# Performance work log

Hardware: AMD Instinct MI355X
Metric: run time of the kernel (lower is better)

## Reference

```python
import jax, jax.numpy as jnp
import numpy as np

D, H, DH, DF = 128, 8, 16, 512
N_Q, N_KV, E = 20000, 20000, 640000


def _xavier(key, shape):
    fan_in, fan_out = shape[1], shape[0]
    lim = float(np.sqrt(6.0 / (fan_in + fan_out)))
    return jax.random.uniform(key, shape, jnp.float32, -lim, lim)


def layer_norm(x, g, b, eps=1e-5):
    mu = jnp.mean(x, axis=-1, keepdims=True)
    var = jnp.var(x, axis=-1, keepdims=True)
    return (x - mu) * jax.lax.rsqrt(var + eps) * g + b


def setup_inputs() -> dict:
    key = jax.random.key(0)
    ks = jax.random.split(key, 12)
    return {
        "q_feat": jax.random.normal(ks[0], (N_Q, D), jnp.float32),
        "kv_feat": jax.random.normal(ks[1], (N_KV, D), jnp.float32),
        "src": jax.random.randint(ks[2], (E,), 0, N_KV, jnp.int32),
        "dst": jax.random.randint(ks[3], (E,), 0, N_Q, jnp.int32),
        "Wq": _xavier(ks[4], (H * DH, D)),
        "Wk": _xavier(ks[5], (H * DH, D)),
        "Wv": _xavier(ks[6], (H * DH, D)),
        "Wo": _xavier(ks[7], (D, H * DH)),
        "W1": _xavier(ks[8], (DF, D)),
        "bf1": jnp.zeros((DF,), jnp.float32),
        "W2": _xavier(ks[9], (D, DF)),
        "bf2": jnp.zeros((D,), jnp.float32),
        "ln1_g": jnp.ones((D,), jnp.float32),
        "ln1_b": jnp.zeros((D,), jnp.float32),
        "ln2_g": jnp.ones((D,), jnp.float32),
        "ln2_b": jnp.zeros((D,), jnp.float32),
    }


def reference(q_feat, kv_feat, src, dst, Wq, Wk, Wv, Wo, W1, bf1, W2, bf2,
              ln1_g, ln1_b, ln2_g, ln2_b):
    n_q = q_feat.shape[0]
    # projections -> [N, H, DH]
    q = (q_feat @ Wq.T).reshape(-1, H, DH)
    k = (kv_feat @ Wk.T).reshape(-1, H, DH)
    v = (kv_feat @ Wv.T).reshape(-1, H, DH)
    # edge scores: u_mul_v then sum over d_head, scaled (score per edge per head)
    score = jnp.einsum('ehd,ehd->eh', k[src], q[dst]) / np.sqrt(DH)
    # edge_softmax grouped by destination node
    mx = jax.ops.segment_max(score, dst, num_segments=n_q)  # [Nq, H]
    ex = jnp.exp(score - mx[dst])
    denom = jax.ops.segment_sum(ex, dst, num_segments=n_q)
    att = ex / denom[dst]  # [E, H]
    # weighted scatter-sum of values to destination nodes
    msg = v[src] * att[:, :, None]  # [E, H, DH]
    out = jax.ops.segment_sum(msg, dst, num_segments=n_q)  # [Nq, H, DH]
    sa = out.reshape(n_q, H * DH) @ Wo.T
    feat = layer_norm(q_feat + sa, ln1_g, ln1_b)
    ff = jax.nn.relu(feat @ W1.T + bf1) @ W2.T + bf2
    return layer_norm(feat + ff, ln2_g, ln2_b)
```

## Files before the change

kernel.cpp:

```cpp
#include <hip/hip_runtime.h>
#include <hip/hip_fp16.h>
#include <math.h>
#include <type_traits>

#define D 128
#define NH 8
#define DHD 16
#define DF 512
#define STR 128

typedef _Float16 half8 __attribute__((ext_vector_type(8)));
typedef _Float16 half4 __attribute__((ext_vector_type(4)));
typedef float f32x4 __attribute__((ext_vector_type(4)));


__global__ __launch_bounds__(256) void mega_kernel(
    const float* __restrict__ q_feat, const float* __restrict__ kv_feat,
    const float* __restrict__ Wq, const float* __restrict__ Wk,
    const float* __restrict__ Wv,
    __half* __restrict__ fq, __half* __restrict__ fkv, int NQ, int NKV,
    const int* __restrict__ dst, const int* __restrict__ src,
    int* __restrict__ cnt, unsigned short* __restrict__ srcg, int E,
    const float* __restrict__ Wo, const float* __restrict__ W1,
    const float* __restrict__ W2,
    __half* __restrict__ wo16, __half* __restrict__ w116, __half* __restrict__ w216) {
    __shared__ __align__(16) __half As[64 * 128];
    __shared__ __align__(16) __half Ws[64 * 128];

    int xt = blockIdx.x;
    int tid = threadIdx.x;

    if (xt >= 2) {
        if (xt == (int)gridDim.x - 1) {
            int g = blockIdx.y * 256 + tid;
            if (g < 36864) {
                const float* s;
                __half* d;
                int idx = g;
                if (idx < 4096) { s = Wo; d = wo16; }
                else if (idx < 20480) { idx -= 4096; s = W1; d = w116; }
                else { idx -= 20480; s = W2; d = w216; }
                float4 f = ((const float4*)s)[idx];
                ushort4 o;
                o.x = __half_as_ushort(__float2half(f.x));
                o.y = __half_as_ushort(__float2half(f.y));
                o.z = __half_as_ushort(__float2half(f.z));
                o.w = __half_as_ushort(__float2half(f.w));
                ((ushort4*)d)[idx] = o;
            }
            return;
        }
        int b = (xt - 2) * gridDim.y + blockIdx.y;
        int i4 = b * 256 + tid;
        int base = i4 << 2;
        if (base < E) {
            int dd[4], ss[4];
            if (base + 3 < E) {
                int4 d4 = ((const int4*)dst)[i4];
                int4 s4 = ((const int4*)src)[i4];
                dd[0] = d4.x; dd[1] = d4.y; dd[2] = d4.z; dd[3] = d4.w;
                ss[0] = s4.x; ss[1] = s4.y; ss[2] = s4.z; ss[3] = s4.w;
#pragma unroll
                for (int u = 0; u < 4; ++u) {
                    int p = atomicAdd(&cnt[dd[u]], 1);
                    if (p < STR) srcg[((size_t)dd[u] << 7) + p] = (unsigned short)ss[u];
                }
            } else {
                for (int u = 0; u < 4 && base + u < E; ++u) {
                    int dn = dst[base + u];
                    int sn = src[base + u];
                    int p = atomicAdd(&cnt[dn], 1);
                    if (p < STR) srcg[((size_t)dn << 7) + p] = (unsigned short)sn;
                }
            }
        }
        return;
    }

    const float* A = xt ? kv_feat : q_feat;
    __half* C = xt ? fkv : fq;
    int O = xt ? 256 : 128;
    int NCT = xt ? 4 : 2;
    int N = xt ? NKV : NQ;
    int row0 = blockIdx.y * 64;
    if (row0 >= N) return;

    int lane = tid & 63;
    int w = tid >> 6;
    int l16 = lane & 15, lq = lane >> 4;

#pragma unroll
    for (int i = 0; i < 4; ++i) {
        int f = tid + i * 256;
        int ln = f & 63;
        int mt = (f >> 6) & 3;
        int kc = f >> 8;
        int m = row0 + mt * 16 + (ln & 15);
        int k = kc * 32 + (ln >> 4) * 8;
        half8 v = {};
        if (m < N) {
            const float4* p = (const float4*)(A + (size_t)m * 128 + k);
            float4 f0 = p[0], f1 = p[1];
            v = (half8){(_Float16)f0.x, (_Float16)f0.y, (_Float16)f0.z, (_Float16)f0.w,
                        (_Float16)f1.x, (_Float16)f1.y, (_Float16)f1.z, (_Float16)f1.w};
        }
        ((half8*)As)[f] = v;
    }

    for (int ct = 0; ct < NCT; ++ct) {
        __syncthreads();
#pragma unroll
        for (int i = 0; i < 4; ++i) {
            int f = tid + i * 256;
            int ln = f & 63;
            int nt = (f >> 6) & 3;
            int kc = f >> 8;
            int n = ct * 64 + nt * 16 + (ln & 15);
            int k = kc * 32 + (ln >> 4) * 8;
            const float* Wsrc;
            int r;
            if (xt == 0) {
                Wsrc = Wq; r = n;
            } else {
                int h = n >> 5, qd = (n >> 3) & 3, isv = (n >> 2) & 1, d2 = n & 3;
                r = h * 16 + qd * 4 + d2;
                Wsrc = isv ? Wv : Wk;
            }
            const float4* p = (const float4*)(Wsrc + (size_t)r * 128 + k);
            float4 f0 = p[0], f1 = p[1];
            ((half8*)Ws)[f] = (half8){(_Float16)f0.x, (_Float16)f0.y, (_Float16)f0.z, (_Float16)f0.w,
                                      (_Float16)f1.x, (_Float16)f1.y, (_Float16)f1.z, (_Float16)f1.w};
        }
        __syncthreads();
        f32x4 acc[4];
#pragma unroll
        for (int j = 0; j < 4; ++j) acc[j] = (f32x4){0.f, 0.f, 0.f, 0.f};
#pragma unroll
        for (int kc = 0; kc < 4; ++kc) {
            half8 a = ((half8*)As)[(kc * 4 + w) * 64 + lane];
            half8 b[4];
#pragma unroll
            for (int j = 0; j < 4; ++j) b[j] = ((half8*)Ws)[(kc * 4 + j) * 64 + lane];
#pragma unroll
            for (int j = 0; j < 4; ++j)
                acc[j] = __builtin_amdgcn_mfma_f32_16x16x32_f16(a, b[j], acc[j], 0, 0, 0);
        }
#pragma unroll
        for (int j = 0; j < 4; ++j) {
            int c = ct * 64 + j * 16 + l16;
#pragma unroll
            for (int r = 0; r < 4; ++r) {
                int row = row0 + w * 16 + lq * 4 + r;
                if (row < N) C[(size_t)row * O + c] = __float2half(acc[j][r]);
            }
        }
    }
}


__global__ __launch_bounds__(256) void attn_kernel(
    const __half* __restrict__ q, const __half* __restrict__ kv,
    const unsigned short* __restrict__ srcg, const int* __restrict__ cnt,
    __half* __restrict__ out, int NQ) {
    int n = blockIdx.x * 4 + (threadIdx.x >> 6);
    if (n >= NQ) return;
    int lane = threadIdx.x & 63;
    int eh = lane >> 5;
    int sub = lane & 31;
    int doff = sub << 2;
    half4 q4 = *(const half4*)(q + (size_t)n * D + doff);
    float q0 = (float)q4[0] * 0.25f, q1 = (float)q4[1] * 0.25f;
    float q2 = (float)q4[2] * 0.25f, q3 = (float)q4[3] * 0.25f;
    int s0 = n << 7;
    int c_ = cnt[n];
    int s1 = s0 + (c_ < STR ? c_ : STR);
    float lA = 0.f, lB = 0.f, lC = 0.f, lD = 0.f;
    f32x4 aA = {0.f, 0.f, 0.f, 0.f}, aB = {0.f, 0.f, 0.f, 0.f};
    f32x4 aC = {0.f, 0.f, 0.f, 0.f}, aD = {0.f, 0.f, 0.f, 0.f};
    int j = s0;
    for (; j + 8 <= s1; j += 8) {
        int e0 = srcg[j + eh];
        int e1 = srcg[j + 2 + eh];
        int e2 = srcg[j + 4 + eh];
        int e3 = srcg[j + 6 + eh];
        half8 c0 = *(const half8*)(kv + (size_t)e0 * 256 + (sub << 3));
        half8 c1 = *(const half8*)(kv + (size_t)e1 * 256 + (sub << 3));
        half8 c2 = *(const half8*)(kv + (size_t)e2 * 256 + (sub << 3));
        half8 c3 = *(const half8*)(kv + (size_t)e3 * 256 + (sub << 3));
        float p0 = q0 * (float)c0[0] + q1 * (float)c0[1] + q2 * (float)c0[2] + q3 * (float)c0[3];
        float p1 = q0 * (float)c1[0] + q1 * (float)c1[1] + q2 * (float)c1[2] + q3 * (float)c1[3];
        float p2 = q0 * (float)c2[0] + q1 * (float)c2[1] + q2 * (float)c2[2] + q3 * (float)c2[3];
        float p3 = q0 * (float)c3[0] + q1 * (float)c3[1] + q2 * (float)c3[2] + q3 * (float)c3[3];
        p0 += __shfl_xor(p0, 1, 4); p0 += __shfl_xor(p0, 2, 4);
        p1 += __shfl_xor(p1, 1, 4); p1 += __shfl_xor(p1, 2, 4);
        p2 += __shfl_xor(p2, 1, 4); p2 += __shfl_xor(p2, 2, 4);
        p3 += __shfl_xor(p3, 1, 4); p3 += __shfl_xor(p3, 2, 4);
        float x0 = __expf(fminf(p0, 70.f));
        float x1 = __expf(fminf(p1, 70.f));
        float x2 = __expf(fminf(p2, 70.f));
        float x3 = __expf(fminf(p3, 70.f));
        lA += x0; lB += x1; lC += x2; lD += x3;
        aA[0] += x0 * (float)c0[4]; aA[1] += x0 * (float)c0[5];
        aA[2] += x0 * (float)c0[6]; aA[3] += x0 * (float)c0[7];
        aB[0] += x1 * (float)c1[4]; aB[1] += x1 * (float)c1[5];
        aB[2] += x1 * (float)c1[6]; aB[3] += x1 * (float)c1[7];
        aC[0] += x2 * (float)c2[4]; aC[1] += x2 * (float)c2[5];
        aC[2] += x2 * (float)c2[6]; aC[3] += x2 * (float)c2[7];
        aD[0] += x3 * (float)c3[4]; aD[1] += x3 * (float)c3[5];
        aD[2] += x3 * (float)c3[6]; aD[3] += x3 * (float)c3[7];
    }
    for (; j + 4 <= s1; j += 4) {
        int e0 = srcg[j + eh];
        int e1 = srcg[j + 2 + eh];
        half8 c0 = *(const half8*)(kv + (size_t)e0 * 256 + (sub << 3));
        half8 c1 = *(const half8*)(kv + (size_t)e1 * 256 + (sub << 3));
        float p0 = q0 * (float)c0[0] + q1 * (float)c0[1] + q2 * (float)c0[2] + q3 * (float)c0[3];
        float p1 = q0 * (float)c1[0] + q1 * (float)c1[1] + q2 * (float)c1[2] + q3 * (float)c1[3];
        p0 += __shfl_xor(p0, 1, 4); p0 += __shfl_xor(p0, 2, 4);
        p1 += __shfl_xor(p1, 1, 4); p1 += __shfl_xor(p1, 2, 4);
        float x0 = __expf(fminf(p0, 70.f));
        float x1 = __expf(fminf(p1, 70.f));
        lA += x0; lB += x1;
        aA[0] += x0 * (float)c0[4]; aA[1] += x0 * (float)c0[5];
        aA[2] += x0 * (float)c0[6]; aA[3] += x0 * (float)c0[7];
        aB[0] += x1 * (float)c1[4]; aB[1] += x1 * (float)c1[5];
        aB[2] += x1 * (float)c1[6]; aB[3] += x1 * (float)c1[7];
    }
    for (; j < s1; j += 2) {
        bool valid = (j + eh) < s1;
        int e0 = srcg[valid ? (j + eh) : s0];
        half8 c0 = *(const half8*)(kv + (size_t)e0 * 256 + (sub << 3));
        float p0 = q0 * (float)c0[0] + q1 * (float)c0[1] + q2 * (float)c0[2] + q3 * (float)c0[3];
        p0 += __shfl_xor(p0, 1, 4); p0 += __shfl_xor(p0, 2, 4);
        float x0 = valid ? __expf(fminf(p0, 70.f)) : 0.f;
        lA += x0;
        aA[0] += x0 * (float)c0[4]; aA[1] += x0 * (float)c0[5];
        aA[2] += x0 * (float)c0[6]; aA[3] += x0 * (float)c0[7];
    }
    float l = (lA + lB) + (lC + lD);
    f32x4 a;
#pragma unroll
    for (int i = 0; i < 4; ++i) a[i] = (aA[i] + aB[i]) + (aC[i] + aD[i]);
    l += __shfl_xor(l, 32);
#pragma unroll
    for (int i = 0; i < 4; ++i) a[i] += __shfl_xor(a[i], 32);
    if (eh == 0) {
        float rl = (l > 0.f) ? 1.f / l : 0.f;
        half4 o = {(_Float16)(a[0] * rl), (_Float16)(a[1] * rl),
                   (_Float16)(a[2] * rl), (_Float16)(a[3] * rl)};
        *(half4*)(out + (size_t)n * D + doff) = o;
    }
}


__device__ __forceinline__ int feat_idx64(int rr, int mt, int c) {
    return (((c >> 5) * 4 + mt) * 64 + ((c >> 3) & 3) * 16 + rr) * 8 + (c & 7);
}

__global__ __launch_bounds__(256) void tail_kernel(
    const __half* __restrict__ A , const __half* __restrict__ Wo16,
    const float* __restrict__ res1 ,
    const float* __restrict__ g1, const float* __restrict__ b1,
    const __half* __restrict__ W1h, const float* __restrict__ fb1,
    const __half* __restrict__ W2h, const float* __restrict__ fb2,
    const float* __restrict__ g2, const float* __restrict__ b2,
    float* __restrict__ out, int N) {
    __shared__ __align__(16) __half Feat[64 * 128];
    __shared__ __align__(16) __half S1[64 * 128];
    __shared__ __align__(16) __half S2[128 * 64];
    __shared__ __align__(16) __half Hs[64 * 64];
    int tid = threadIdx.x, lane = tid & 63, w = tid >> 6;
    int row0 = blockIdx.x * 64;
    int l16 = lane & 15, lq = lane >> 4;

#pragma unroll
    for (int i = 0; i < 4; ++i) {
        int f = tid + i * 256;
        int ln = f & 63, mt = (f >> 6) & 3, kc = f >> 8;
        int m = row0 + mt * 16 + (ln & 15);
        int k = kc * 32 + (ln >> 4) * 8;
        half8 av = {};
        if (m < N) av = *(const half8*)(A + (size_t)m * D + k);
        ((half8*)S1)[f] = av;
    }

    f32x4 acc[8];
#pragma unroll
    for (int j = 0; j < 8; ++j) acc[j] = (f32x4){0.f, 0.f, 0.f, 0.f};
#pragma unroll
    for (int kt = 0; kt < 2; ++kt) {
        __syncthreads();
#pragma unroll
        for (int i = 0; i < 4; ++i) {
            int f = tid + i * 256;
            int ln = f & 63, ot = (f >> 6) & 7, kc2 = f >> 9;
            int o = ot * 16 + (ln & 15);
            int k = kt * 64 + kc2 * 32 + (ln >> 4) * 8;
            ((half8*)S2)[f] = *(const half8*)(Wo16 + (size_t)o * D + k);
        }
        __syncthreads();
#pragma unroll
        for (int kc2 = 0; kc2 < 2; ++kc2) {
            half8 a = ((half8*)S1)[((kt * 2 + kc2) * 4 + w) * 64 + lane];
            half8 bf[8];
#pragma unroll
            for (int j = 0; j < 8; ++j) bf[j] = ((half8*)S2)[(kc2 * 8 + j) * 64 + lane];
#pragma unroll
            for (int j = 0; j < 8; ++j)
                acc[j] = __builtin_amdgcn_mfma_f32_16x16x32_f16(a, bf[j], acc[j], 0, 0, 0);
        }
    }
    __syncthreads();

#pragma unroll
    for (int r = 0; r < 4; ++r) {
        int rr = lq * 4 + r;
        int row = row0 + w * 16 + rr;
        bool valid = row < N;
        float vals[8];
        float s = 0.f, sq = 0.f;
#pragma unroll
        for (int j = 0; j < 8; ++j) {
            int c = j * 16 + l16;
            float v = acc[j][r];
            if (valid) v += res1[(size_t)row * D + c];
            vals[j] = v;
            s += v;
            sq += v * v;
        }
#pragma unroll
        for (int m = 1; m < 16; m <<= 1) {
            s += __shfl_xor(s, m, 16);
            sq += __shfl_xor(sq, m, 16);
        }
        float mu = s * (1.f / 128.f);
        float var = sq * (1.f / 128.f) - mu * mu;
        float inv = rsqrtf(var + 1e-5f);
#pragma unroll
        for (int j = 0; j < 8; ++j) {
            int c = j * 16 + l16;
            float o = (vals[j] - mu) * inv * g1[c] + b1[c];
            Feat[feat_idx64(rr, w, c)] = __float2half(o);
        }
    }
    __syncthreads();

    half8 a_all[4];
#pragma unroll
    for (int kc = 0; kc < 4; ++kc)
        a_all[kc] = ((half8*)Feat)[(kc * 4 + w) * 64 + lane];

    f32x4 oacc[8];
#pragma unroll
    for (int j = 0; j < 8; ++j) oacc[j] = (f32x4){0.f, 0.f, 0.f, 0.f};

    for (int hc = 0; hc < 8; ++hc) {
        __syncthreads();
#pragma unroll
        for (int i = 0; i < 4; ++i) {
            int f = tid + i * 256;
            int ln = f & 63, nt = (f >> 6) & 3, kc = f >> 8;
            int n = hc * 64 + nt * 16 + (ln & 15);
            int k = kc * 32 + (ln >> 4) * 8;
            ((half8*)S1)[f] = *(const half8*)(W1h + (size_t)n * D + k);
        }
#pragma unroll
        for (int i = 0; i < 4; ++i) {
            int f = tid + i * 256;
            int ln = f & 63, ot = (f >> 6) & 7, kc2 = f >> 9;
            int o = ot * 16 + (ln & 15);
            int k = hc * 64 + kc2 * 32 + (ln >> 4) * 8;
            ((half8*)S2)[f] = *(const half8*)(W2h + (size_t)o * DF + k);
        }
        __syncthreads();
        f32x4 hacc[4];
#pragma unroll
        for (int j = 0; j < 4; ++j) hacc[j] = (f32x4){0.f, 0.f, 0.f, 0.f};
#pragma unroll
        for (int kc = 0; kc < 4; ++kc) {
            half8 b[4];
#pragma unroll
            for (int j = 0; j < 4; ++j) b[j] = ((half8*)S1)[(kc * 4 + j) * 64 + lane];
#pragma unroll
            for (int j = 0; j < 4; ++j)
                hacc[j] = __builtin_amdgcn_mfma_f32_16x16x32_f16(a_all[kc], b[j], hacc[j], 0, 0, 0);
        }
#pragma unroll
        for (int j = 0; j < 4; ++j) {
            float bias1 = fb1[hc * 64 + j * 16 + l16];
#pragma unroll
            for (int r = 0; r < 4; ++r) {
                float v = fmaxf(hacc[j][r] + bias1, 0.f);
                int kc2 = j >> 1;
                int lanep = ((j & 1) * 2 + (l16 >> 3)) * 16 + lq * 4 + r;
                Hs[((kc2 * 4 + w) * 64 + lanep) * 8 + (l16 & 7)] = __float2half(v);
            }
        }
        __syncthreads();
#pragma unroll
        for (int kc2 = 0; kc2 < 2; ++kc2) {
            half8 a = ((half8*)Hs)[(kc2 * 4 + w) * 64 + lane];
            half8 b[8];
#pragma unroll
            for (int ot = 0; ot < 8; ++ot) b[ot] = ((half8*)S2)[(kc2 * 8 + ot) * 64 + lane];
#pragma unroll
            for (int ot = 0; ot < 8; ++ot)
                oacc[ot] = __builtin_amdgcn_mfma_f32_16x16x32_f16(a, b[ot], oacc[ot], 0, 0, 0);
        }
    }

#pragma unroll
    for (int r = 0; r < 4; ++r) {
        int rr = lq * 4 + r;
        int row = row0 + w * 16 + rr;
        bool valid = row < N;
        float vals[8];
        float s = 0.f, sq = 0.f;
#pragma unroll
        for (int j = 0; j < 8; ++j) {
            int c = j * 16 + l16;
            float v = oacc[j][r] + fb2[c] + __half2float(Feat[feat_idx64(rr, w, c)]);
            vals[j] = v;
            s += v;
            sq += v * v;
        }
#pragma unroll
        for (int m = 1; m < 16; m <<= 1) {
            s += __shfl_xor(s, m, 16);
            sq += __shfl_xor(sq, m, 16);
        }
        float mu = s * (1.f / 128.f);
        float var = sq * (1.f / 128.f) - mu * mu;
        float inv = rsqrtf(var + 1e-5f);
        if (valid) {
#pragma unroll
            for (int j = 0; j < 8; ++j) {
                int c = j * 16 + l16;
                out[(size_t)row * D + c] = (vals[j] - mu) * inv * g2[c] + b2[c];
            }
        }
    }
}


extern "C" void kernel_launch(void* const* d_in, const int* in_sizes, int n_in,
                              void* d_out, int out_size, void* d_ws, size_t ws_size,
                              hipStream_t stream) {
    const float* q_feat = (const float*)d_in[0];
    const float* kv_feat = (const float*)d_in[1];
    const int* src = (const int*)d_in[2];
    const int* dst = (const int*)d_in[3];
    const float* Wq = (const float*)d_in[4];
    const float* Wk = (const float*)d_in[5];
    const float* Wv = (const float*)d_in[6];
    const float* Wo = (const float*)d_in[7];
    const float* W1 = (const float*)d_in[8];
    const float* bf1 = (const float*)d_in[9];
    const float* W2 = (const float*)d_in[10];
    const float* bf2 = (const float*)d_in[11];
    const float* ln1g = (const float*)d_in[12];
    const float* ln1b = (const float*)d_in[13];
    const float* ln2g = (const float*)d_in[14];
    const float* ln2b = (const float*)d_in[15];

    int NQ = in_sizes[0] / D;
    int NKV = in_sizes[1] / D;
    int E = in_sizes[2];
    float* out = (float*)d_out;

    char* base = (char*)d_ws;
    size_t off = 0;
    auto alloc = [&](size_t bytes) -> void* {
        void* p = base + off;
        off += (bytes + 255) & ~(size_t)255;
        return p;
    };
    __half* fq16 = (__half*)alloc((size_t)NQ * D * 2);
    __half* fkv = (__half*)alloc((size_t)NKV * 256 * 2);
    __half* fattn16 = (__half*)alloc((size_t)NQ * D * 2);
    int* cnt = (int*)alloc((size_t)NQ * 4);
    unsigned short* srcg = (unsigned short*)alloc((size_t)NQ * STR * 2);
    __half* wo16 = (__half*)alloc((size_t)D * D * 2);
    __half* w116 = (__half*)alloc((size_t)DF * D * 2);
    __half* w216 = (__half*)alloc((size_t)D * DF * 2);

    hipMemsetAsync(cnt, 0, (size_t)NQ * sizeof(int), stream);

    dim3 blk(256);
    int NMX = NQ > NKV ? NQ : NKV;
    int ytiles = (NMX + 63) / 64;
    int fillBlocks = (E + 1023) / 1024;
    int fillPlanes = (fillBlocks + ytiles - 1) / ytiles;
    mega_kernel<<<dim3(3 + fillPlanes, ytiles), blk, 0, stream>>>(
        q_feat, kv_feat, Wq, Wk, Wv, fq16, fkv, NQ, NKV,
        dst, src, cnt, srcg, E, Wo, W1, W2, wo16, w116, w216);

    attn_kernel<<<(NQ + 3) / 4, blk, 0, stream>>>(fq16, fkv, srcg, cnt, fattn16, NQ);

    tail_kernel<<<(NQ + 63) / 64, blk, 0, stream>>>(
        fattn16, wo16, q_feat, ln1g, ln1b, w116, bf1, w216, bf2, ln2g, ln2b, out, NQ);
}
```

Measured before the change: 213.1 us.

## Shard edge bucketing counters across eight sub-slots to reduce atomic contention

The per-destination atomic counter and source list are split into 8 shards chosen by fill block, each holding up to 32 entries. This spreads atomics on the same destination across separate addresses. The attention kernel first gathers the shard lists into a per-wave shared-memory list, then runs the same online accumulation from LDS. The cost is eight counter reads per node, a larger memset and srcg buffer, and tighter per-shard capacity, which could drop edges for skewed degree distributions.

```diff
diff --git a/kernel.cpp b/kernel.cpp
--- a/kernel.cpp
+++ b/kernel.cpp
@@ -7,7 +7,8 @@
 #define NH 8
 #define DHD 16
 #define DF 512
-#define STR 128
+#define NSH 8
+#define SSL 32
 
 typedef _Float16 half8 __attribute__((ext_vector_type(8)));
 typedef _Float16 half4 __attribute__((ext_vector_type(4)));
@@ -51,26 +52,28 @@
             return;
         }
         int b = (xt - 2) * gridDim.y + blockIdx.y;
+        int sh = (blockIdx.y * gridDim.x + blockIdx.x) & (NSH - 1);
         int i4 = b * 256 + tid;
         int base = i4 << 2;
         if (base < E) {
-            int dd[4], ss[4];
             if (base + 3 < E) {
                 int4 d4 = ((const int4*)dst)[i4];
                 int4 s4 = ((const int4*)src)[i4];
-                dd[0] = d4.x; dd[1] = d4.y; dd[2] = d4.z; dd[3] = d4.w;
-                ss[0] = s4.x; ss[1] = s4.y; ss[2] = s4.z; ss[3] = s4.w;
+                int dd[4] = {d4.x, d4.y, d4.z, d4.w};
+                int ss[4] = {s4.x, s4.y, s4.z, s4.w};
 #pragma unroll
                 for (int u = 0; u < 4; ++u) {
-                    int p = atomicAdd(&cnt[dd[u]], 1);
-                    if (p < STR) srcg[((size_t)dd[u] << 7) + p] = (unsigned short)ss[u];
+                    int p = atomicAdd(&cnt[sh * NQ + dd[u]], 1);
+                    if (p < SSL)
+                        srcg[((size_t)dd[u] << 8) + (sh << 5) + p] = (unsigned short)ss[u];
                 }
             } else {
                 for (int u = 0; u < 4 && base + u < E; ++u) {
                     int dn = dst[base + u];
                     int sn = src[base + u];
-                    int p = atomicAdd(&cnt[dn], 1);
-                    if (p < STR) srcg[((size_t)dn << 7) + p] = (unsigned short)sn;
+                    int p = atomicAdd(&cnt[sh * NQ + dn], 1);
+                    if (p < SSL)
+                        srcg[((size_t)dn << 8) + (sh << 5) + p] = (unsigned short)sn;
                 }
             }
         }
@@ -162,27 +165,38 @@
     const __half* __restrict__ q, const __half* __restrict__ kv,
     const unsigned short* __restrict__ srcg, const int* __restrict__ cnt,
     __half* __restrict__ out, int NQ) {
-    int n = blockIdx.x * 4 + (threadIdx.x >> 6);
+    __shared__ unsigned short list[4][NSH * SSL];
+    int wv = threadIdx.x >> 6;
+    int n = blockIdx.x * 4 + wv;
     if (n >= NQ) return;
     int lane = threadIdx.x & 63;
     int eh = lane >> 5;
     int sub = lane & 31;
     int doff = sub << 2;
+
+    int t0 = 0;
+#pragma unroll
+    for (int r = 0; r < NSH; ++r) {
+        int cr = cnt[r * NQ + n];
+        cr = cr < SSL ? cr : SSL;
+        if (lane < cr)
+            list[wv][t0 + lane] = srcg[((size_t)n << 8) + (r << 5) + lane];
+        t0 += cr;
+    }
+    int total = t0;
+
     half4 q4 = *(const half4*)(q + (size_t)n * D + doff);
     float q0 = (float)q4[0] * 0.25f, q1 = (float)q4[1] * 0.25f;
     float q2 = (float)q4[2] * 0.25f, q3 = (float)q4[3] * 0.25f;
-    int s0 = n << 7;
-    int c_ = cnt[n];
-    int s1 = s0 + (c_ < STR ? c_ : STR);
     float lA = 0.f, lB = 0.f, lC = 0.f, lD = 0.f;
     f32x4 aA = {0.f, 0.f, 0.f, 0.f}, aB = {0.f, 0.f, 0.f, 0.f};
     f32x4 aC = {0.f, 0.f, 0.f, 0.f}, aD = {0.f, 0.f, 0.f, 0.f};
-    int j = s0;
-    for (; j + 8 <= s1; j += 8) {
-        int e0 = srcg[j + eh];
-        int e1 = srcg[j + 2 + eh];
-        int e2 = srcg[j + 4 + eh];
-        int e3 = srcg[j + 6 + eh];
+    int j = 0;
+    for (; j + 8 <= total; j += 8) {
+        int e0 = list[wv][j + eh];
+        int e1 = list[wv][j + 2 + eh];
+        int e2 = list[wv][j + 4 + eh];
+        int e3 = list[wv][j + 6 + eh];
         half8 c0 = *(const half8*)(kv + (size_t)e0 * 256 + (sub << 3));
         half8 c1 = *(const half8*)(kv + (size_t)e1 * 256 + (sub << 3));
         half8 c2 = *(const half8*)(kv + (size_t)e2 * 256 + (sub << 3));
@@ -209,9 +223,9 @@
         aD[0] += x3 * (float)c3[4]; aD[1] += x3 * (float)c3[5];
         aD[2] += x3 * (float)c3[6]; aD[3] += x3 * (float)c3[7];
     }
-    for (; j + 4 <= s1; j += 4) {
-        int e0 = srcg[j + eh];
-        int e1 = srcg[j + 2 + eh];
+    for (; j + 4 <= total; j += 4) {
+        int e0 = list[wv][j + eh];
+        int e1 = list[wv][j + 2 + eh];
         half8 c0 = *(const half8*)(kv + (size_t)e0 * 256 + (sub << 3));
         half8 c1 = *(const half8*)(kv + (size_t)e1 * 256 + (sub << 3));
         float p0 = q0 * (float)c0[0] + q1 * (float)c0[1] + q2 * (float)c0[2] + q3 * (float)c0[3];
@@ -226,9 +240,9 @@
         aB[0] += x1 * (float)c1[4]; aB[1] += x1 * (float)c1[5];
         aB[2] += x1 * (float)c1[6]; aB[3] += x1 * (float)c1[7];
     }
-    for (; j < s1; j += 2) {
-        bool valid = (j + eh) < s1;
-        int e0 = srcg[valid ? (j + eh) : s0];
+    for (; j < total; j += 2) {
+        bool valid = (j + eh) < total;
+        int e0 = list[wv][valid ? (j + eh) : 0];
         half8 c0 = *(const half8*)(kv + (size_t)e0 * 256 + (sub << 3));
         float p0 = q0 * (float)c0[0] + q1 * (float)c0[1] + q2 * (float)c0[2] + q3 * (float)c0[3];
         p0 += __shfl_xor(p0, 1, 4); p0 += __shfl_xor(p0, 2, 4);
@@ -478,13 +492,13 @@
     __half* fq16 = (__half*)alloc((size_t)NQ * D * 2);
     __half* fkv = (__half*)alloc((size_t)NKV * 256 * 2);
     __half* fattn16 = (__half*)alloc((size_t)NQ * D * 2);
-    int* cnt = (int*)alloc((size_t)NQ * 4);
-    unsigned short* srcg = (unsigned short*)alloc((size_t)NQ * STR * 2);
+    int* cnt = (int*)alloc((size_t)NSH * NQ * 4);
+    unsigned short* srcg = (unsigned short*)alloc((size_t)NQ * NSH * SSL * 2);
     __half* wo16 = (__half*)alloc((size_t)D * D * 2);
     __half* w116 = (__half*)alloc((size_t)DF * D * 2);
     __half* w216 = (__half*)alloc((size_t)D * DF * 2);
 
-    hipMemsetAsync(cnt, 0, (size_t)NQ * sizeof(int), stream);
+    hipMemsetAsync(cnt, 0, (size_t)NSH * NQ * sizeof(int), stream);
 
     dim3 blk(256);
     int NMX = NQ > NKV ? NQ : NKV;
```

Result: slower. 218.2 us (+2.4%).
